# Optimization experiments

Hardware: AMD Instinct MI355X
Metric: run time of the kernel (lower is better)

The kernel has to match this reference:

```python
import jax, jax.numpy as jnp
import numpy as np

D = 768
H = 16
DH = D // H  # 48


def setup_inputs() -> dict:
    key = jax.random.key(0)
    ks = jax.random.split(key, 7)
    s = 0.02
    x = jax.random.normal(ks[0], (4, 2048, D), dtype=jnp.float32)
    # weights stored as (in, out); torch Linear is y = x @ W.T + b
    W_qkv = jax.random.normal(ks[1], (D, 3 * D), dtype=jnp.float32) * s
    b_qkv = jax.random.normal(ks[2], (3 * D,), dtype=jnp.float32) * s
    W_o = jax.random.normal(ks[3], (D, D), dtype=jnp.float32) * s
    b_o = jax.random.normal(ks[4], (D,), dtype=jnp.float32) * s
    W_p = jax.random.normal(ks[5], (D, D), dtype=jnp.float32) * s
    b_p = jax.random.normal(ks[6], (D,), dtype=jnp.float32) * s
    return {"x": x, "W_qkv": W_qkv, "b_qkv": b_qkv, "W_o": W_o, "b_o": b_o, "W_p": W_p, "b_p": b_p}


def reference(x, W_qkv, b_qkv, W_o, b_o, W_p, b_p):
    b, n, _ = x.shape
    qkv = x @ W_qkv + b_qkv                     # (b, n, 3*D)
    # reshape to (b, n, H, 3*DH) as in torch, then chunk last dim into q,k,v
    # -> per-head interleaved layout [q_h | k_h | v_h]
    qkv = qkv.reshape(b, n, H, 3, DH).transpose(0, 2, 1, 3, 4)  # (b, H, n, 3, DH)
    q, k, v = qkv[..., 0, :], qkv[..., 1, :], qkv[..., 2, :]    # (b, H, n, DH)
    alpha = jnp.einsum("bhqd,bhkd->bhqk", q, k) / jnp.sqrt(jnp.float32(DH))
    alpha = jax.nn.softmax(alpha, axis=-1)      # dropout: eval mode (identity)
    out = jnp.einsum("bhqk,bhkd->bhqd", alpha, v)
    out = out.transpose(0, 2, 1, 3).reshape(b, n, D)
    out = out @ W_o + b_o
    out = out @ W_p + b_p
    return out
```

## Files before the change

kernel.cpp:

```cpp
#include <hip/hip_runtime.h>

#define DEV __device__ __forceinline__

typedef __attribute__((ext_vector_type(4))) float f32x4;
typedef __attribute__((ext_vector_type(8))) short bf16x8;
typedef __attribute__((ext_vector_type(4))) short bf16x4;
typedef __attribute__((ext_vector_type(4))) unsigned int u32x4;

DEV short f2bf(float f) {
  union { float f; unsigned u; } c; c.f = f;
  unsigned r = c.u + 0x7FFFu + ((c.u >> 16) & 1u);
  return (short)(r >> 16);
}

DEV unsigned cvtpk(float lo, float hi) {
  unsigned r;
  asm("v_cvt_pk_bf16_f32 %0, %1, %2" : "=v"(r) : "v"(lo), "v"(hi));
  return r;
}

DEV float exp2r(float x) { return __builtin_amdgcn_exp2f(x); }

DEV void gl_lds16(short* lds, const short* g) {
  __builtin_amdgcn_global_load_lds(
      (__attribute__((address_space(1))) void*)(void*)g,
      (__attribute__((address_space(3))) void*)lds, 16, 0, 0);
}

DEV int xcd_swz(int orig, int nwg) {
  int q = nwg >> 3, r = nwg & 7;
  int xcd = orig & 7, idx = orig >> 3;
  return (xcd < r ? xcd * (q + 1) : r * (q + 1) + (xcd - r) * q) + idx;
}

__global__ __launch_bounds__(256) void k_cvt(const float* __restrict__ in, short* __restrict__ out) {
  int i = blockIdx.x * 256 + threadIdx.x;
  float4 v = reinterpret_cast<const float4*>(in)[i];
  bf16x4 o;
  o[0] = f2bf(v.x); o[1] = f2bf(v.y); o[2] = f2bf(v.z); o[3] = f2bf(v.w);
  reinterpret_cast<bf16x4*>(out)[i] = o;
}

__global__ __launch_bounds__(256) void k_tcvt(const float* __restrict__ W, short* __restrict__ WT,
                                              int Kd, int Nd) {
  __shared__ float t[32][33];
  int nb = blockIdx.x * 32, kb = blockIdx.y * 32;
  int tx = threadIdx.x, ty = threadIdx.y;
#pragma unroll
  for (int i = ty; i < 32; i += 8) t[i][tx] = W[(long)(kb + i) * Nd + nb + tx];
  __syncthreads();
#pragma unroll
  for (int i = ty; i < 32; i += 8) WT[(long)(nb + i) * Kd + kb + tx] = f2bf(t[tx][i]);
}

__global__ __launch_bounds__(256) void k_bias(const float* __restrict__ bo, const float* __restrict__ bp,
                                              const float* __restrict__ Wp, float* __restrict__ bc) {
  int j = blockIdx.x * 256 + threadIdx.x;
  int k0 = blockIdx.y * 48;
  float s = 0.f;
#pragma unroll
  for (int k = 0; k < 48; ++k) s += bo[k0 + k] * Wp[(long)(k0 + k) * 768 + j];
  if (blockIdx.y == 0) s += bp[j];
  atomicAdd(&bc[j], s);
}

template <int MODE>
__global__ __launch_bounds__(256) void k_gemm(
    const short* __restrict__ A, const short* __restrict__ BT, const float* __restrict__ bias,
    short* __restrict__ Cb, float* __restrict__ Cf,
    short* __restrict__ Qp, short* __restrict__ Kp, short* __restrict__ VT,
    int M, int N, int K) {
  __shared__ short As[3][128 * 32];
  __shared__ short Bs[3][128 * 32];
  const int tid = threadIdx.x;
  const int w = tid >> 6, lane = tid & 63;
  const int lr = lane & 15, g = lane >> 4;

  const int nbx = gridDim.x;
  int lin = blockIdx.y * nbx + blockIdx.x;
  lin = xcd_swz(lin, nbx * gridDim.y);
  const int bx = lin % nbx, by = lin / nbx;
  const int m0 = by * 128, n0 = bx * 128;
  const int wm = (w >> 1) * 64, wn = (w & 1) * 64;

  f32x4 acc[4][4];
#pragma unroll
  for (int i = 0; i < 4; ++i)
#pragma unroll
    for (int j = 0; j < 4; ++j)
#pragma unroll
      for (int r = 0; r < 4; ++r) acc[i][j][r] = 0.f;

  const short* Ab = A + (long)m0 * K;
  const short* Bb = BT + (long)n0 * K;
  const int row_s = tid >> 2;
  const int c_s = tid & 3;
  const int nk = K >> 5;

  auto STAGE = [&](int b, int kt) {
    const int k0 = kt << 5;
#pragma unroll
    for (int i = 0; i < 2; ++i) {
      int row = row_s + i * 64;
      int cs = c_s ^ ((row >> 1) & 3);
      gl_lds16(&As[b][(i * 256 + w * 64) * 8], Ab + (long)row * K + k0 + cs * 8);
      gl_lds16(&Bs[b][(i * 256 + w * 64) * 8], Bb + (long)row * K + k0 + cs * 8);
    }
  };

  STAGE(0, 0);
  STAGE(1, 1);

  for (int kt = 0; kt < nk; ++kt) {
    if (kt < nk - 1) asm volatile("s_waitcnt vmcnt(4)" ::: "memory");
    else             asm volatile("s_waitcnt vmcnt(0)" ::: "memory");
    __builtin_amdgcn_s_barrier();

    if (kt + 2 < nk) STAGE((kt + 2) % 3, kt + 2);

    const short* AsC = As[kt % 3];
    const short* BsC = Bs[kt % 3];
    bf16x8 af[4], bf[4];
#pragma unroll
    for (int mi = 0; mi < 4; ++mi) {
      int r = wm + mi * 16 + lr;
      int c = g ^ ((r >> 1) & 3);
      af[mi] = *reinterpret_cast<const bf16x8*>(AsC + r * 32 + c * 8);
    }
#pragma unroll
    for (int nj = 0; nj < 4; ++nj) {
      int r = wn + nj * 16 + lr;
      int c = g ^ ((r >> 1) & 3);
      bf[nj] = *reinterpret_cast<const bf16x8*>(BsC + r * 32 + c * 8);
    }
    __builtin_amdgcn_s_setprio(1);
#pragma unroll
    for (int mi = 0; mi < 4; ++mi)
#pragma unroll
      for (int nj = 0; nj < 4; ++nj)
        acc[mi][nj] = __builtin_amdgcn_mfma_f32_16x16x32_bf16(af[mi], bf[nj], acc[mi][nj], 0, 0, 0);
    __builtin_amdgcn_s_setprio(0);
  }

#pragma unroll
  for (int nj = 0; nj < 4; ++nj) {
    int col = n0 + wn + nj * 16 + lr;
    float bv = (MODE == 3) ? 0.f : bias[col];
    if (MODE == 0) {
      int h = col / 144;
      int rem = col - h * 144;
      int s = rem / 48;
      int d = rem - s * 48;
#pragma unroll
      for (int mi = 0; mi < 4; ++mi)
#pragma unroll
        for (int r = 0; r < 4; ++r) {
          int row = m0 + wm + mi * 16 + g * 4 + r;
          float val = acc[mi][nj][r] + bv;
          int b = row >> 11, n = row & 2047;
          int bh = (b << 4) + h;
          if (s == 0) {
            long o = ((long)(bh * 2048 + n)) * 64 + d;
            Qp[o] = f2bf(val * 0.20823051649867783f);
            if (d < 16) Qp[o + 48] = 0;
          } else if (s == 1) {
            long o = ((long)(bh * 2048 + n)) * 64 + d;
            Kp[o] = f2bf(val);
            if (d < 16) Kp[o + 48] = 0;
          } else {
            VT[((long)(bh * 48 + d)) * 2048 + n] = f2bf(val);
          }
        }
    } else {
#pragma unroll
      for (int mi = 0; mi < 4; ++mi)
#pragma unroll
        for (int r = 0; r < 4; ++r) {
          int row = m0 + wm + mi * 16 + g * 4 + r;
          float val = acc[mi][nj][r] + bv;
          if (MODE == 2) Cf[(long)row * N + col] = val;
          else           Cb[(long)row * N + col] = f2bf(val);
        }
    }
  }
}

__global__ __launch_bounds__(256, 4) void k_attn(const short* __restrict__ Q, const short* __restrict__ K,
                                                 const short* __restrict__ VT, short* __restrict__ AO) {
  const int tid = threadIdx.x, w = tid >> 6, lane = tid & 63;
  const int lr = lane & 15, g = lane >> 4;
  const int orig = blockIdx.x;
  const int logical = (orig & 7) * 128 + (orig >> 3);
  const int bh = logical >> 4;
  const int q0 = (logical & 15) * 128 + w * 32;

  const short* Qh = Q + (long)bh * 2048 * 64;
  const short* Kh = K + (long)bh * 2048 * 64;
  const short* VTh = VT + (long)bh * 48 * 2048;

  __shared__ short Ks[2][64 * 64];
  __shared__ short Vs[2][48 * 64];

  const int r_l = lane >> 3, c_l = lane & 7;
  const int gc8 = (c_l ^ r_l) * 8;

  bf16x8 bq0 = *reinterpret_cast<const bf16x8*>(Qh + (q0 + lr) * 64 + g * 8);
  bf16x8 bq1 = *reinterpret_cast<const bf16x8*>(Qh + (q0 + lr) * 64 + 32 + g * 8);
  bf16x8 bq2 = *reinterpret_cast<const bf16x8*>(Qh + (q0 + 16 + lr) * 64 + g * 8);
  bf16x8 bq3 = *reinterpret_cast<const bf16x8*>(Qh + (q0 + 16 + lr) * 64 + 32 + g * 8);

  bf16x8 vones;
#pragma unroll
  for (int i = 0; i < 8; ++i) vones[i] = (short)0x3F80;

  f32x4 accA[3], accB[3];
#pragma unroll
  for (int df = 0; df < 3; ++df)
#pragma unroll
    for (int r = 0; r < 4; ++r) { accA[df][r] = 0.f; accB[df][r] = 0.f; }
  f32x4 acclA = {0.f, 0.f, 0.f, 0.f}, acclB = {0.f, 0.f, 0.f, 0.f};

  const short* kg = Kh + (long)(w * 8 + r_l) * 64 + gc8;
  const short* vg = VTh + (long)(w * 8 + r_l) * 2048 + gc8;

  auto STAGE = [&](int b) {
    gl_lds16(&Ks[b][w * 512], kg);
    gl_lds16(&Ks[b][(w + 4) * 512], kg + 2048);
    gl_lds16(&Vs[b][w * 512], vg);
    if (w < 2) gl_lds16(&Vs[b][(w + 4) * 512], vg + 65536);
  };

  STAGE(0);
  kg += 4096; vg += 64;
  asm volatile("s_waitcnt vmcnt(0)" ::: "memory");
  __syncthreads();

  const int sw = lr & 7;
  const int goff = (g & 1) * 4;
  const int ghalf = g >> 1;

  for (int t = 0; t < 32; ++t) {
    const int cur = t & 1;
    if (t < 31) {
      STAGE(cur ^ 1);
      kg += 4096; vg += 64;
    }

    const short* KsC = Ks[cur];
    const short* VsC = Vs[cur];

    f32x4 stA[4], stB[4];
    __builtin_amdgcn_s_setprio(1);
#pragma unroll
    for (int kf = 0; kf < 4; ++kf) {
      const short* kr = KsC + (kf * 16 + lr) * 64;
      bf16x8 a0 = *reinterpret_cast<const bf16x8*>(kr + (g ^ sw) * 8);
      bf16x8 a1 = *reinterpret_cast<const bf16x8*>(kr + ((4 + g) ^ sw) * 8);
      f32x4 sA = {0.f, 0.f, 0.f, 0.f}, sB = {0.f, 0.f, 0.f, 0.f};
      sA = __builtin_amdgcn_mfma_f32_16x16x32_bf16(a0, bq0, sA, 0, 0, 0);
      sB = __builtin_amdgcn_mfma_f32_16x16x32_bf16(a0, bq2, sB, 0, 0, 0);
      sA = __builtin_amdgcn_mfma_f32_16x16x32_bf16(a1, bq1, sA, 0, 0, 0);
      sB = __builtin_amdgcn_mfma_f32_16x16x32_bf16(a1, bq3, sB, 0, 0, 0);
      stA[kf] = sA; stB[kf] = sB;
    }
    __builtin_amdgcn_s_setprio(0);

#pragma unroll
    for (int kf = 0; kf < 4; ++kf)
#pragma unroll
      for (int r = 0; r < 4; ++r) {
        stA[kf][r] = exp2r(stA[kf][r]);
        stB[kf][r] = exp2r(stB[kf][r]);
      }

    __builtin_amdgcn_s_setprio(1);
#pragma unroll
    for (int ks = 0; ks < 2; ++ks) {
      u32x4 bwA, bwB;
      bwA[0] = cvtpk(stA[2 * ks][0], stA[2 * ks][1]);
      bwA[1] = cvtpk(stA[2 * ks][2], stA[2 * ks][3]);
      bwA[2] = cvtpk(stA[2 * ks + 1][0], stA[2 * ks + 1][1]);
      bwA[3] = cvtpk(stA[2 * ks + 1][2], stA[2 * ks + 1][3]);
      bwB[0] = cvtpk(stB[2 * ks][0], stB[2 * ks][1]);
      bwB[1] = cvtpk(stB[2 * ks][2], stB[2 * ks][3]);
      bwB[2] = cvtpk(stB[2 * ks + 1][0], stB[2 * ks + 1][1]);
      bwB[3] = cvtpk(stB[2 * ks + 1][2], stB[2 * ks + 1][3]);
      bf16x8 bpA = __builtin_bit_cast(bf16x8, bwA);
      bf16x8 bpB = __builtin_bit_cast(bf16x8, bwB);
      const int off_lo = ((ks * 4 + ghalf) ^ sw) * 8 + goff;
      const int off_hi = ((ks * 4 + 2 + ghalf) ^ sw) * 8 + goff;
      acclA = __builtin_amdgcn_mfma_f32_16x16x32_bf16(vones, bpA, acclA, 0, 0, 0);
      acclB = __builtin_amdgcn_mfma_f32_16x16x32_bf16(vones, bpB, acclB, 0, 0, 0);
#pragma unroll
      for (int df = 0; df < 3; ++df) {
        const short* vbase = VsC + (df * 16 + lr) * 64;
        union { bf16x8 v; bf16x4 h[2]; } av;
        av.h[0] = *reinterpret_cast<const bf16x4*>(vbase + off_lo);
        av.h[1] = *reinterpret_cast<const bf16x4*>(vbase + off_hi);
        accA[df] = __builtin_amdgcn_mfma_f32_16x16x32_bf16(av.v, bpA, accA[df], 0, 0, 0);
        accB[df] = __builtin_amdgcn_mfma_f32_16x16x32_bf16(av.v, bpB, accB[df], 0, 0, 0);
      }
    }
    __builtin_amdgcn_s_setprio(0);

    asm volatile("s_waitcnt vmcnt(0)" ::: "memory");
    __syncthreads();
  }

  int b = bh >> 4, h = bh & 15;
  float invA = 1.f / acclA[0];
  float invB = 1.f / acclB[0];
  long rowA = ((long)((b << 11) + q0 + lr)) * 768 + h * 48;
  long rowB = ((long)((b << 11) + q0 + 16 + lr)) * 768 + h * 48;
#pragma unroll
  for (int df = 0; df < 3; ++df) {
    bf16x4 oA, oB;
#pragma unroll
    for (int r = 0; r < 4; ++r) { oA[r] = f2bf(accA[df][r] * invA); oB[r] = f2bf(accB[df][r] * invB); }
    *reinterpret_cast<bf16x4*>(AO + rowA + df * 16 + g * 4) = oA;
    *reinterpret_cast<bf16x4*>(AO + rowB + df * 16 + g * 4) = oB;
  }
}

extern "C" void kernel_launch(void* const* d_in, const int* in_sizes, int n_in,
                              void* d_out, int out_size, void* d_ws, size_t ws_size,
                              hipStream_t stream) {
  const float* x    = (const float*)d_in[0];
  const float* Wqkv = (const float*)d_in[1];
  const float* bqkv = (const float*)d_in[2];
  const float* Wo   = (const float*)d_in[3];
  const float* bo   = (const float*)d_in[4];
  const float* Wp   = (const float*)d_in[5];
  const float* bp   = (const float*)d_in[6];

  char* ws = (char*)d_ws;
  short* xb    = (short*)(ws + 0);
  short* WqkvT = (short*)(ws + 12582912);
  short* WpT   = (short*)(ws + 17301504);
  short* Qp    = (short*)(ws + 18481152);
  short* Kp    = (short*)(ws + 35258368);
  short* VT    = (short*)(ws + 52035584);
  short* AO    = (short*)(ws + 64618496);
  short* Wob   = (short*)(ws + 0);
  short* WoWpT = (short*)(ws + 2097152);
  float* bc    = (float*)(ws + 4194304);

  k_cvt<<<6144, 256, 0, stream>>>(x, xb);
  k_tcvt<<<dim3(72, 24), dim3(32, 8), 0, stream>>>(Wqkv, WqkvT, 768, 2304);
  k_tcvt<<<dim3(24, 24), dim3(32, 8), 0, stream>>>(Wp, WpT, 768, 768);

  k_gemm<0><<<dim3(18, 64), 256, 0, stream>>>(xb, WqkvT, bqkv, nullptr, nullptr,
                                              Qp, Kp, VT, 8192, 2304, 768);
  k_cvt<<<576, 256, 0, stream>>>(Wo, Wob);
  k_gemm<3><<<dim3(6, 6), 256, 0, stream>>>(WpT, Wob, nullptr, WoWpT, nullptr,
                                            nullptr, nullptr, nullptr, 768, 768, 768);
  hipMemsetAsync(bc, 0, 768 * sizeof(float), stream);
  k_bias<<<dim3(3, 16), 256, 0, stream>>>(bo, bp, Wp, bc);

  k_attn<<<1024, 256, 0, stream>>>(Qp, Kp, VT, AO);
  k_gemm<2><<<dim3(6, 64), 256, 0, stream>>>(AO, WoWpT, bc, nullptr, (float*)d_out,
                                             nullptr, nullptr, nullptr, 8192, 768, 768);
}
```

Measured before the change: 183.9 us.

## Add 256x128 BK=64 QKV GEMM kernel and merge x and Wo conversions

```diff
diff --git a/kernel.cpp b/kernel.cpp
--- a/kernel.cpp
+++ b/kernel.cpp
@@ -33,8 +33,12 @@
   return (xcd < r ? xcd * (q + 1) : r * (q + 1) + (xcd - r) * q) + idx;
 }
 
-__global__ __launch_bounds__(256) void k_cvt(const float* __restrict__ in, short* __restrict__ out) {
-  int i = blockIdx.x * 256 + threadIdx.x;
+__global__ __launch_bounds__(256) void k_cvt2(const float* __restrict__ in1, short* __restrict__ out1,
+                                              int nb1, const float* __restrict__ in2, short* __restrict__ out2) {
+  int b = blockIdx.x;
+  const float* in = in1; short* out = out1;
+  if (b >= nb1) { in = in2; out = out2; b -= nb1; }
+  int i = b * 256 + threadIdx.x;
   float4 v = reinterpret_cast<const float4*>(in)[i];
   bf16x4 o;
   o[0] = f2bf(v.x); o[1] = f2bf(v.y); o[2] = f2bf(v.z); o[3] = f2bf(v.w);
@@ -64,12 +68,128 @@
   atomicAdd(&bc[j], s);
 }
 
+__global__ __launch_bounds__(512, 1) void k_gemm8(
+    const short* __restrict__ A, const short* __restrict__ BT, const float* __restrict__ bias,
+    short* __restrict__ Qp, short* __restrict__ Kp, short* __restrict__ VT, int K) {
+  __shared__ short As[2][256 * 64];
+  __shared__ short Bs[2][128 * 64];
+  const int tid = threadIdx.x;
+  const int w = tid >> 6, lane = tid & 63;
+  const int lr = lane & 15, g = lane >> 4;
+  const int r_l = lane >> 3, c_l = lane & 7;
+  const int gsw = (c_l ^ r_l) * 8;
+
+  const int nbx = gridDim.x;
+  int lin = blockIdx.y * nbx + blockIdx.x;
+  lin = xcd_swz(lin, nbx * gridDim.y);
+  const int bx = lin % nbx, by = lin / nbx;
+  const int m0 = by * 256, n0 = bx * 128;
+  const int wm = (w >> 1) * 64, wn = (w & 1) * 64;
+
+  f32x4 acc[4][4];
+#pragma unroll
+  for (int i = 0; i < 4; ++i)
+#pragma unroll
+    for (int j = 0; j < 4; ++j)
+#pragma unroll
+      for (int r = 0; r < 4; ++r) acc[i][j][r] = 0.f;
+
+  const short* Ab = A + (long)m0 * K;
+  const short* Bb = BT + (long)n0 * K;
+  const int nk = K >> 6;
+
+  auto STAGE_A = [&](int s, int kt, int j) {
+    int rowb = j * 64 + w * 8;
+    gl_lds16(&As[s][rowb * 64], Ab + (long)(rowb + r_l) * K + (kt << 6) + gsw);
+  };
+  auto STAGE_B = [&](int s, int kt, int j) {
+    int rowb = j * 64 + w * 8;
+    gl_lds16(&Bs[s][rowb * 64], Bb + (long)(rowb + r_l) * K + (kt << 6) + gsw);
+  };
+
+  STAGE_A(0, 0, 0); STAGE_A(0, 0, 1); STAGE_A(0, 0, 2); STAGE_A(0, 0, 3);
+  STAGE_B(0, 0, 0); STAGE_B(0, 0, 1);
+
+  for (int kt = 0; kt < nk; ++kt) {
+    const int cur = kt & 1, ns = cur ^ 1;
+    const bool pre = (kt + 1 < nk);
+    asm volatile("s_waitcnt vmcnt(0)" ::: "memory");
+    __builtin_amdgcn_s_barrier();
+
+    const short* AsC = As[cur];
+    const short* BsC = Bs[cur];
+
+    bf16x8 bf[4][2];
+    bf16x8 af[2];
+#pragma unroll
+    for (int p = 0; p < 4; ++p) {
+      if (p == 0) {
+#pragma unroll
+        for (int nj = 0; nj < 4; ++nj) {
+          int r = wn + nj * 16 + lr;
+          const short* rb = BsC + r * 64;
+          bf[nj][0] = *reinterpret_cast<const bf16x8*>(rb + ((0 + g) ^ (r & 7)) * 8);
+          bf[nj][1] = *reinterpret_cast<const bf16x8*>(rb + ((4 + g) ^ (r & 7)) * 8);
+        }
+      }
+      {
+        int r = wm + p * 16 + lr;
+        const short* ra = AsC + r * 64;
+        af[0] = *reinterpret_cast<const bf16x8*>(ra + ((0 + g) ^ (r & 7)) * 8);
+        af[1] = *reinterpret_cast<const bf16x8*>(ra + ((4 + g) ^ (r & 7)) * 8);
+      }
+      if (pre) {
+        if (p == 0)      { STAGE_A(ns, kt + 1, 0); STAGE_A(ns, kt + 1, 1); }
+        else if (p == 1) { STAGE_A(ns, kt + 1, 2); STAGE_A(ns, kt + 1, 3); }
+        else if (p == 2) { STAGE_B(ns, kt + 1, 0); STAGE_B(ns, kt + 1, 1); }
+      }
+      __builtin_amdgcn_s_barrier();
+      __builtin_amdgcn_s_setprio(1);
+#pragma unroll
+      for (int nj = 0; nj < 4; ++nj) {
+        acc[p][nj] = __builtin_amdgcn_mfma_f32_16x16x32_bf16(af[0], bf[nj][0], acc[p][nj], 0, 0, 0);
+        acc[p][nj] = __builtin_amdgcn_mfma_f32_16x16x32_bf16(af[1], bf[nj][1], acc[p][nj], 0, 0, 0);
+      }
+      __builtin_amdgcn_s_setprio(0);
+      if (p < 3) __builtin_amdgcn_s_barrier();
+    }
+  }
+
+#pragma unroll
+  for (int nj = 0; nj < 4; ++nj) {
+    int col = n0 + wn + nj * 16 + lr;
+    float bv = bias[col];
+    int h = col / 144;
+    int rem = col - h * 144;
+    int s = rem / 48;
+    int d = rem - s * 48;
+#pragma unroll
+    for (int mi = 0; mi < 4; ++mi)
+#pragma unroll
+      for (int r = 0; r < 4; ++r) {
+        int row = m0 + wm + mi * 16 + g * 4 + r;
+        float val = acc[mi][nj][r] + bv;
+        int b = row >> 11, n = row & 2047;
+        int bh = (b << 4) + h;
+        if (s == 0) {
+          long o = ((long)(bh * 2048 + n)) * 64 + d;
+          Qp[o] = f2bf(val * 0.20823051649867783f);
+          if (d < 16) Qp[o + 48] = 0;
+        } else if (s == 1) {
+          long o = ((long)(bh * 2048 + n)) * 64 + d;
+          Kp[o] = f2bf(val);
+          if (d < 16) Kp[o + 48] = 0;
+        } else {
+          VT[((long)(bh * 48 + d)) * 2048 + n] = f2bf(val);
+        }
+      }
+  }
+}
+
 template <int MODE>
 __global__ __launch_bounds__(256) void k_gemm(
     const short* __restrict__ A, const short* __restrict__ BT, const float* __restrict__ bias,
-    short* __restrict__ Cb, float* __restrict__ Cf,
-    short* __restrict__ Qp, short* __restrict__ Kp, short* __restrict__ VT,
-    int M, int N, int K) {
+    short* __restrict__ Cb, float* __restrict__ Cf, int M, int N, int K) {
   __shared__ short As[3][128 * 32];
   __shared__ short Bs[3][128 * 32];
   const int tid = threadIdx.x;
@@ -146,42 +266,15 @@
   for (int nj = 0; nj < 4; ++nj) {
     int col = n0 + wn + nj * 16 + lr;
     float bv = (MODE == 3) ? 0.f : bias[col];
-    if (MODE == 0) {
-      int h = col / 144;
-      int rem = col - h * 144;
-      int s = rem / 48;
-      int d = rem - s * 48;
-#pragma unroll
-      for (int mi = 0; mi < 4; ++mi)
-#pragma unroll
-        for (int r = 0; r < 4; ++r) {
-          int row = m0 + wm + mi * 16 + g * 4 + r;
-          float val = acc[mi][nj][r] + bv;
-          int b = row >> 11, n = row & 2047;
-          int bh = (b << 4) + h;
-          if (s == 0) {
-            long o = ((long)(bh * 2048 + n)) * 64 + d;
-            Qp[o] = f2bf(val * 0.20823051649867783f);
-            if (d < 16) Qp[o + 48] = 0;
-          } else if (s == 1) {
-            long o = ((long)(bh * 2048 + n)) * 64 + d;
-            Kp[o] = f2bf(val);
-            if (d < 16) Kp[o + 48] = 0;
-          } else {
-            VT[((long)(bh * 48 + d)) * 2048 + n] = f2bf(val);
-          }
-        }
-    } else {
-#pragma unroll
-      for (int mi = 0; mi < 4; ++mi)
-#pragma unroll
-        for (int r = 0; r < 4; ++r) {
-          int row = m0 + wm + mi * 16 + g * 4 + r;
-          float val = acc[mi][nj][r] + bv;
-          if (MODE == 2) Cf[(long)row * N + col] = val;
-          else           Cb[(long)row * N + col] = f2bf(val);
-        }
-    }
+#pragma unroll
+    for (int mi = 0; mi < 4; ++mi)
+#pragma unroll
+      for (int r = 0; r < 4; ++r) {
+        int row = m0 + wm + mi * 16 + g * 4 + r;
+        float val = acc[mi][nj][r] + bv;
+        if (MODE == 2) Cf[(long)row * N + col] = val;
+        else           Cb[(long)row * N + col] = f2bf(val);
+      }
   }
 }
 
@@ -336,28 +429,25 @@
   char* ws = (char*)d_ws;
   short* xb    = (short*)(ws + 0);
   short* WqkvT = (short*)(ws + 12582912);
+  short* Wob   = (short*)(ws + 16121856);
   short* WpT   = (short*)(ws + 17301504);
   short* Qp    = (short*)(ws + 18481152);
   short* Kp    = (short*)(ws + 35258368);
   short* VT    = (short*)(ws + 52035584);
   short* AO    = (short*)(ws + 64618496);
-  short* Wob   = (short*)(ws + 0);
   short* WoWpT = (short*)(ws + 2097152);
   float* bc    = (float*)(ws + 4194304);
 
-  k_cvt<<<6144, 256, 0, stream>>>(x, xb);
+  k_cvt2<<<6720, 256, 0, stream>>>(x, xb, 6144, Wo, Wob);
   k_tcvt<<<dim3(72, 24), dim3(32, 8), 0, stream>>>(Wqkv, WqkvT, 768, 2304);
   k_tcvt<<<dim3(24, 24), dim3(32, 8), 0, stream>>>(Wp, WpT, 768, 768);
 
-  k_gemm<0><<<dim3(18, 64), 256, 0, stream>>>(xb, WqkvT, bqkv, nullptr, nullptr,
-                                              Qp, Kp, VT, 8192, 2304, 768);
-  k_cvt<<<576, 256, 0, stream>>>(Wo, Wob);
-  k_gemm<3><<<dim3(6, 6), 256, 0, stream>>>(WpT, Wob, nullptr, WoWpT, nullptr,
-                                            nullptr, nullptr, nullptr, 768, 768, 768);
+  k_gemm8<<<dim3(18, 32), 512, 0, stream>>>(xb, WqkvT, bqkv, Qp, Kp, VT, 768);
+
+  k_gemm<3><<<dim3(6, 6), 256, 0, stream>>>(WpT, Wob, nullptr, WoWpT, nullptr, 768, 768, 768);
   hipMemsetAsync(bc, 0, 768 * sizeof(float), stream);
   k_bias<<<dim3(3, 16), 256, 0, stream>>>(bo, bp, Wp, bc);
 
   k_attn<<<1024, 256, 0, stream>>>(Qp, Kp, VT, AO);
-  k_gemm<2><<<dim3(6, 64), 256, 0, stream>>>(AO, WoWpT, bc, nullptr, (float*)d_out,
-                                             nullptr, nullptr, nullptr, 8192, 768, 768);
-}
+  k_gemm<2><<<dim3(6, 64), 256, 0, stream>>>(AO, WoWpT, bc, nullptr, (float*)d_out, 8192, 768, 768);
+}
```

New measurement: 196.6 us. 1.07x slower.
